# Kernel optimization log

Hardware: AMD Instinct MI355X
Metric: run time of the kernel (lower is better)

Reference implementation:

```python
import jax, jax.numpy as jnp
import numpy as np

IN_F = 8192
OUT_F = 8192
R = 16
LORA_ALPHA = 32
BLOCK = 64
SCALING = LORA_ALPHA / R  # 2.0
NUMEL = IN_F * OUT_F


def dequantize_4bit(packed, scales):
    # packed: [numel//2] bytes (stored as int32 in [0,255]); element 2i = low nibble, 2i+1 = high nibble
    low = packed & 0xF
    high = (packed >> 4) & 0xF
    q = jnp.stack([low, high], axis=-1).reshape(-1)          # [numel] ints in [0,15]
    flat = q.astype(jnp.float32) - 8.0                        # signed 4-bit
    flat = (flat.reshape(-1, BLOCK) * scales[:, None]).reshape(-1)  # blockwise scale
    return flat.reshape(OUT_F, IN_F)


def setup_inputs() -> dict:
    key = jax.random.key(0)
    k1, k2, k3, k4, k5 = jax.random.split(key, 5)
    x = jax.random.normal(k1, (1, 64, IN_F), dtype=jnp.float32)
    packed_weights = jax.random.randint(k2, (NUMEL // 2,), 0, 256, dtype=jnp.int32)
    block_scales = jax.random.uniform(k3, (NUMEL // BLOCK,), dtype=jnp.float32) * 0.05
    # kaiming_uniform(a=sqrt(5)) on [R, IN_F] -> bound = 1/sqrt(IN_F)
    bound = 1.0 / np.sqrt(IN_F)
    lora_A = jax.random.uniform(k4, (R, IN_F), minval=-bound, maxval=bound, dtype=jnp.float32)
    # original init is zeros; use small randn for a non-trivial baseline
    lora_B = jax.random.normal(k5, (OUT_F, R), dtype=jnp.float32) * 0.02
    return {"x": x, "packed_weights": packed_weights, "block_scales": block_scales,
            "lora_A": lora_A, "lora_B": lora_B}


def reference(x, packed_weights, block_scales, lora_A, lora_B):
    W = dequantize_4bit(packed_weights, block_scales).astype(x.dtype)  # [OUT_F, IN_F]
    base_out = jnp.einsum('bsi,oi->bso', x, W)                         # no bias (bias_buffer=None)
    lora_out = jnp.einsum('bsr,or->bso', jnp.einsum('bsi,ri->bsr', x, lora_A), lora_B) * SCALING
    return base_out + lora_out
```

## Files before the change

kernel.cpp:

```cpp
#include <hip/hip_runtime.h>
#include <hip/hip_bf16.h>

#define IN_F 8192
#define OUT_F 8192
#define SEQ 64
#define LORA_R 16

typedef __attribute__((ext_vector_type(4))) float f32x4;
typedef __attribute__((ext_vector_type(4))) int i32x4;
typedef __attribute__((ext_vector_type(8))) unsigned short u16x8;
typedef __attribute__((ext_vector_type(4))) unsigned short u16x4;
typedef _Float16 f16x2 __attribute__((ext_vector_type(2)));
typedef _Float16 f16x8 __attribute__((ext_vector_type(8)));

typedef __attribute__((address_space(3))) unsigned int lds_u32;
typedef const __attribute__((address_space(1))) unsigned int glb_u32;

__device__ __forceinline__ void gl_lds16(const void* g, void* l) {
    __builtin_amdgcn_global_load_lds((glb_u32*)g, (lds_u32*)l, 16, 0, 0);
}

__global__ __launch_bounds__(256) void k_prep(
    const float* __restrict__ x, const float* __restrict__ A,
    unsigned short* __restrict__ xb, float* __restrict__ t) {
    __shared__ float part[64];
    const int s = blockIdx.x >> 1, p = blockIdx.x & 1;
    const int w = threadIdx.x >> 6, lane = threadIdx.x & 63;
    const int kbase = p * 4096 + w * 1024;
    const float* xr = x + s * IN_F + kbase;

    f32x4 xv[4];
    #pragma unroll
    for (int j = 0; j < 4; ++j) {
        xv[j] = *(const f32x4*)(xr + j * 256 + lane * 4);
        u16x4 h;
        h[0] = __builtin_bit_cast(unsigned short, (_Float16)xv[j].x);
        h[1] = __builtin_bit_cast(unsigned short, (_Float16)xv[j].y);
        h[2] = __builtin_bit_cast(unsigned short, (_Float16)xv[j].z);
        h[3] = __builtin_bit_cast(unsigned short, (_Float16)xv[j].w);
        *(u16x4*)(xb + s * IN_F + kbase + j * 256 + lane * 4) = h;
    }

    float acc[LORA_R];
    #pragma unroll
    for (int r = 0; r < LORA_R; ++r) acc[r] = 0.f;
    #pragma unroll
    for (int r = 0; r < LORA_R; ++r) {
        const float* ar = A + r * IN_F + kbase;
        #pragma unroll
        for (int j = 0; j < 4; ++j) {
            f32x4 av = *(const f32x4*)(ar + j * 256 + lane * 4);
            acc[r] = fmaf(xv[j].x, av.x, acc[r]);
            acc[r] = fmaf(xv[j].y, av.y, acc[r]);
            acc[r] = fmaf(xv[j].z, av.z, acc[r]);
            acc[r] = fmaf(xv[j].w, av.w, acc[r]);
        }
    }
    #pragma unroll
    for (int r = 0; r < LORA_R; ++r) {
        float v = acc[r];
        #pragma unroll
        for (int off = 32; off; off >>= 1) v += __shfl_down(v, off, 64);
        if (lane == 0) part[w * 16 + r] = v;
    }
    __syncthreads();
    if (threadIdx.x < 16)
        t[s * 32 + p * 16 + threadIdx.x] = part[threadIdx.x] + part[16 + threadIdx.x] +
                                           part[32 + threadIdx.x] + part[48 + threadIdx.x];
}

__global__ __launch_bounds__(512, 2) void k_main(
    const int* __restrict__ packed, const float* __restrict__ scales,
    const unsigned short* __restrict__ xb, const float* __restrict__ t,
    const float* __restrict__ B, float* __restrict__ out) {
    __shared__ char lds[90624];
    _Float16* xs = (_Float16*)lds;
    int* wt = (int*)(lds + 49152);
    float* scs = (float*)(lds + 73728);
    float* accs = (float*)lds;

    const int tid = threadIdx.x;
    const int n0 = blockIdx.x * 32;
    const int w = tid >> 6, lane = tid & 63;
    const int nh = w >> 2, wkk = w & 3;
    const int q = lane >> 4, c16 = lane & 15;

    const int lrow = lane >> 4, lcol = lane & 15;
    const int xr0 = w * 8 + lrow, xr1 = xr0 + 4;
    const int wr  = w * 4 + lrow;
    const unsigned short* xg0 = xb + (size_t)xr0 * IN_F + ((lcol ^ (xr0 & 7)) << 3);
    const unsigned short* xg1 = xb + (size_t)xr1 * IN_F + ((lcol ^ (xr1 & 7)) << 3);
    const int* wgp = packed + (long)(n0 + wr) * (IN_F / 2) + ((lcol ^ (wr & 7)) << 2);

    _Float16* xd0 = xs + w * 8 * 128;
    _Float16* xd1 = xd0 + 4 * 128;
    int* wd = wt + w * 256;

    {
        int row = tid >> 4, g = tid & 15;
        const float* sp = scales + (n0 + row) * (IN_F / 64);
        *(f32x4*)(scs + row * 132 + g * 4)      = *(const f32x4*)(sp + g * 4);
        *(f32x4*)(scs + row * 132 + 64 + g * 4) = *(const f32x4*)(sp + 64 + g * 4);
    }

    f32x4 acc[4];
    #pragma unroll
    for (int mt = 0; mt < 4; ++mt) acc[mt] = (f32x4){0.f, 0.f, 0.f, 0.f};

    const int pvo = (nh * 16 + c16) * 64 + ((wkk * 16 + q * 4) ^ ((c16 & 7) << 2));
    int afo[4];
    #pragma unroll
    for (int mt = 0; mt < 4; ++mt)
        afo[mt] = (mt * 16 + c16) * 128 + ((wkk * 32 + q * 8) ^ ((c16 & 7) << 3));
    const int sco = (nh * 16 + c16) * 132 + (wkk >> 1);

    asm volatile("s_waitcnt lgkmcnt(0)" ::: "memory");
    __builtin_amdgcn_s_barrier();

    gl_lds16(xg0, xd0);
    gl_lds16(xg1, xd1);
    gl_lds16(wgp, wd);
    gl_lds16(xg0 + 128, xd0 + 8192);
    gl_lds16(xg1 + 128, xd1 + 8192);
    gl_lds16(wgp + 64,  wd + 2048);

    const f16x2 c1032 = {(_Float16)1032.0f, (_Float16)1032.0f};

    int cur = 0, nxt = 2;
    for (int kt = 0; kt < 64; ++kt) {
        if (kt < 63) asm volatile("s_waitcnt vmcnt(3)" ::: "memory");
        else         asm volatile("s_waitcnt vmcnt(0)" ::: "memory");
        __builtin_amdgcn_s_barrier();
        __builtin_amdgcn_sched_barrier(0);
        if (kt < 62) {
            const size_t xoff = (size_t)(kt + 2) * 128;
            gl_lds16(xg0 + xoff, xd0 + nxt * 8192);
            gl_lds16(xg1 + xoff, xd1 + nxt * 8192);
            gl_lds16(wgp + (kt + 2) * 64, wd + nxt * 2048);
        }
        i32x4 pv = *(const i32x4*)(wt + cur * 2048 + pvo);
        float scf = scs[sco + kt * 2];
        _Float16 sch = (_Float16)scf;
        f16x2 sc2 = {sch, sch};
        f16x8 bf;
        #pragma unroll
        for (int m = 0; m < 4; ++m) {
            unsigned u = ((((unsigned)pv[m] << 12) | (unsigned)pv[m]) & 0x000F000Fu) | 0x64006400u;
            f16x2 h = __builtin_bit_cast(f16x2, u);
            h = (h - c1032) * sc2;
            bf[2 * m] = h.x;
            bf[2 * m + 1] = h.y;
        }
        const _Float16* xbase = xs + cur * 8192;
        #pragma unroll
        for (int mt = 0; mt < 4; ++mt) {
            f16x8 af = *(const f16x8*)(xbase + afo[mt]);
            acc[mt] = __builtin_amdgcn_mfma_f32_16x16x32_f16(af, bf, acc[mt], 0, 0, 0);
        }
        cur = (cur == 2) ? 0 : cur + 1;
        nxt = (nxt == 2) ? 0 : nxt + 1;
    }
    __syncthreads();

    float* myacc = accs + w * (64 * 17);
    #pragma unroll
    for (int mt = 0; mt < 4; ++mt)
        #pragma unroll
        for (int r = 0; r < 4; ++r)
            myacc[(mt * 16 + q * 4 + r) * 17 + c16] = acc[mt][r];
    __syncthreads();

    #pragma unroll
    for (int j = 0; j < 4; ++j) {
        int p = tid + j * 512;
        int s = p >> 5, c = p & 31;
        const float* ab = accs + (c >> 4) * 4 * (64 * 17) + s * 17 + (c & 15);
        float v = ab[0] + ab[64 * 17] + ab[2 * 64 * 17] + ab[3 * 64 * 17];
        const float* tp = t + s * 32;
        const float* bp = B + (n0 + c) * LORA_R;
        f32x4 t0 = *(const f32x4*)tp        + *(const f32x4*)(tp + 16);
        f32x4 t1 = *(const f32x4*)(tp + 4)  + *(const f32x4*)(tp + 20);
        f32x4 t2 = *(const f32x4*)(tp + 8)  + *(const f32x4*)(tp + 24);
        f32x4 t3 = *(const f32x4*)(tp + 12) + *(const f32x4*)(tp + 28);
        f32x4 b0 = *(const f32x4*)bp,       b1 = *(const f32x4*)(bp + 4);
        f32x4 b2 = *(const f32x4*)(bp + 8), b3 = *(const f32x4*)(bp + 12);
        float lr = t0.x * b0.x + t0.y * b0.y + t0.z * b0.z + t0.w * b0.w
                 + t1.x * b1.x + t1.y * b1.y + t1.z * b1.z + t1.w * b1.w
                 + t2.x * b2.x + t2.y * b2.y + t2.z * b2.z + t2.w * b2.w
                 + t3.x * b3.x + t3.y * b3.y + t3.z * b3.z + t3.w * b3.w;
        v += 2.0f * lr;
        out[s * OUT_F + n0 + c] = v;
    }
}

extern "C" void kernel_launch(void* const* d_in, const int* in_sizes, int n_in,
                              void* d_out, int out_size, void* d_ws, size_t ws_size,
                              hipStream_t stream) {
    const float* x      = (const float*)d_in[0];
    const int* packed   = (const int*)d_in[1];
    const float* scales = (const float*)d_in[2];
    const float* lora_A = (const float*)d_in[3];
    const float* lora_B = (const float*)d_in[4];
    float* out = (float*)d_out;

    unsigned short* xb = (unsigned short*)d_ws;
    float* t = (float*)((char*)d_ws + (size_t)SEQ * IN_F * 2);

    k_prep<<<128, 256, 0, stream>>>(x, lora_A, xb, t);
    k_main<<<256, 512, 0, stream>>>(packed, scales, xb, t, lora_B, out);
}
```

Before: 221.0 us.

## Deepen main-loop prefetch to four LDS stages and split LoRA prep across more blocks

```diff
diff --git a/kernel.cpp b/kernel.cpp
--- a/kernel.cpp
+++ b/kernel.cpp
@@ -24,14 +24,14 @@
     const float* __restrict__ x, const float* __restrict__ A,
     unsigned short* __restrict__ xb, float* __restrict__ t) {
     __shared__ float part[64];
-    const int s = blockIdx.x >> 1, p = blockIdx.x & 1;
+    const int s = blockIdx.x >> 2, p = blockIdx.x & 3;
     const int w = threadIdx.x >> 6, lane = threadIdx.x & 63;
-    const int kbase = p * 4096 + w * 1024;
+    const int kbase = p * 2048 + w * 512;
     const float* xr = x + s * IN_F + kbase;
 
-    f32x4 xv[4];
-    #pragma unroll
-    for (int j = 0; j < 4; ++j) {
+    f32x4 xv[2];
+    #pragma unroll
+    for (int j = 0; j < 2; ++j) {
         xv[j] = *(const f32x4*)(xr + j * 256 + lane * 4);
         u16x4 h;
         h[0] = __builtin_bit_cast(unsigned short, (_Float16)xv[j].x);
@@ -48,7 +48,7 @@
     for (int r = 0; r < LORA_R; ++r) {
         const float* ar = A + r * IN_F + kbase;
         #pragma unroll
-        for (int j = 0; j < 4; ++j) {
+        for (int j = 0; j < 2; ++j) {
             f32x4 av = *(const f32x4*)(ar + j * 256 + lane * 4);
             acc[r] = fmaf(xv[j].x, av.x, acc[r]);
             acc[r] = fmaf(xv[j].y, av.y, acc[r]);
@@ -65,7 +65,7 @@
     }
     __syncthreads();
     if (threadIdx.x < 16)
-        t[s * 32 + p * 16 + threadIdx.x] = part[threadIdx.x] + part[16 + threadIdx.x] +
+        t[s * 64 + p * 16 + threadIdx.x] = part[threadIdx.x] + part[16 + threadIdx.x] +
                                            part[32 + threadIdx.x] + part[48 + threadIdx.x];
 }
 
@@ -73,11 +73,12 @@
     const int* __restrict__ packed, const float* __restrict__ scales,
     const unsigned short* __restrict__ xb, const float* __restrict__ t,
     const float* __restrict__ B, float* __restrict__ out) {
-    __shared__ char lds[90624];
+    __shared__ char lds[115200];
     _Float16* xs = (_Float16*)lds;
-    int* wt = (int*)(lds + 49152);
-    float* scs = (float*)(lds + 73728);
+    int* wt = (int*)(lds + 65536);
+    float* scs = (float*)(lds + 98304);
     float* accs = (float*)lds;
+    float* tred = scs;
 
     const int tid = threadIdx.x;
     const int n0 = blockIdx.x * 32;
@@ -117,26 +118,28 @@
     asm volatile("s_waitcnt lgkmcnt(0)" ::: "memory");
     __builtin_amdgcn_s_barrier();
 
-    gl_lds16(xg0, xd0);
-    gl_lds16(xg1, xd1);
-    gl_lds16(wgp, wd);
-    gl_lds16(xg0 + 128, xd0 + 8192);
-    gl_lds16(xg1 + 128, xd1 + 8192);
-    gl_lds16(wgp + 64,  wd + 2048);
+    #pragma unroll
+    for (int c = 0; c < 3; ++c) {
+        gl_lds16(xg0 + (size_t)c * 128, xd0 + c * 8192);
+        gl_lds16(xg1 + (size_t)c * 128, xd1 + c * 8192);
+        gl_lds16(wgp + c * 64,          wd  + c * 2048);
+    }
 
     const f16x2 c1032 = {(_Float16)1032.0f, (_Float16)1032.0f};
 
-    int cur = 0, nxt = 2;
     for (int kt = 0; kt < 64; ++kt) {
-        if (kt < 63) asm volatile("s_waitcnt vmcnt(3)" ::: "memory");
-        else         asm volatile("s_waitcnt vmcnt(0)" ::: "memory");
+        if (kt < 62)       asm volatile("s_waitcnt vmcnt(6)" ::: "memory");
+        else if (kt == 62) asm volatile("s_waitcnt vmcnt(3)" ::: "memory");
+        else               asm volatile("s_waitcnt vmcnt(0)" ::: "memory");
         __builtin_amdgcn_s_barrier();
         __builtin_amdgcn_sched_barrier(0);
-        if (kt < 62) {
-            const size_t xoff = (size_t)(kt + 2) * 128;
+        const int cur = kt & 3;
+        if (kt < 61) {
+            const int nxt = (kt + 3) & 3;
+            const size_t xoff = (size_t)(kt + 3) * 128;
             gl_lds16(xg0 + xoff, xd0 + nxt * 8192);
             gl_lds16(xg1 + xoff, xd1 + nxt * 8192);
-            gl_lds16(wgp + (kt + 2) * 64, wd + nxt * 2048);
+            gl_lds16(wgp + (kt + 3) * 64, wd + nxt * 2048);
         }
         i32x4 pv = *(const i32x4*)(wt + cur * 2048 + pvo);
         float scf = scs[sco + kt * 2];
@@ -157,8 +160,6 @@
             f16x8 af = *(const f16x8*)(xbase + afo[mt]);
             acc[mt] = __builtin_amdgcn_mfma_f32_16x16x32_f16(af, bf, acc[mt], 0, 0, 0);
         }
-        cur = (cur == 2) ? 0 : cur + 1;
-        nxt = (nxt == 2) ? 0 : nxt + 1;
     }
     __syncthreads();
 
@@ -168,6 +169,12 @@
         #pragma unroll
         for (int r = 0; r < 4; ++r)
             myacc[(mt * 16 + q * 4 + r) * 17 + c16] = acc[mt][r];
+    #pragma unroll
+    for (int jj = 0; jj < 2; ++jj) {
+        int p2 = tid + jj * 512;
+        const float* tp = t + (p2 >> 4) * 64 + (p2 & 15);
+        tred[p2] = tp[0] + tp[16] + tp[32] + tp[48];
+    }
     __syncthreads();
 
     #pragma unroll
@@ -176,12 +183,10 @@
         int s = p >> 5, c = p & 31;
         const float* ab = accs + (c >> 4) * 4 * (64 * 17) + s * 17 + (c & 15);
         float v = ab[0] + ab[64 * 17] + ab[2 * 64 * 17] + ab[3 * 64 * 17];
-        const float* tp = t + s * 32;
+        const float* trow = tred + s * 16;
         const float* bp = B + (n0 + c) * LORA_R;
-        f32x4 t0 = *(const f32x4*)tp        + *(const f32x4*)(tp + 16);
-        f32x4 t1 = *(const f32x4*)(tp + 4)  + *(const f32x4*)(tp + 20);
-        f32x4 t2 = *(const f32x4*)(tp + 8)  + *(const f32x4*)(tp + 24);
-        f32x4 t3 = *(const f32x4*)(tp + 12) + *(const f32x4*)(tp + 28);
+        f32x4 t0 = *(const f32x4*)trow,        t1 = *(const f32x4*)(trow + 4);
+        f32x4 t2 = *(const f32x4*)(trow + 8),  t3 = *(const f32x4*)(trow + 12);
         f32x4 b0 = *(const f32x4*)bp,       b1 = *(const f32x4*)(bp + 4);
         f32x4 b2 = *(const f32x4*)(bp + 8), b3 = *(const f32x4*)(bp + 12);
         float lr = t0.x * b0.x + t0.y * b0.y + t0.z * b0.z + t0.w * b0.w
@@ -206,6 +211,6 @@
     unsigned short* xb = (unsigned short*)d_ws;
     float* t = (float*)((char*)d_ws + (size_t)SEQ * IN_F * 2);
 
-    k_prep<<<128, 256, 0, stream>>>(x, lora_A, xb, t);
+    k_prep<<<256, 256, 0, stream>>>(x, lora_A, xb, t);
     k_main<<<256, 512, 0, stream>>>(packed, scales, xb, t, lora_B, out);
 }
```

After: 217.1 us. No clear change (-1.8%).
